# Kernel optimization log

Measured on AMD Instinct MI355X. Metric: run time of the kernel, lower is better.

Reference implementation:

```python
import jax, jax.numpy as jnp
import numpy as np

B, S, H, F, E, TOPK = 2, 1024, 1024, 2816, 8, 2

def setup_inputs() -> dict:
    key = jax.random.key(0)
    k1, k2, k3, k4 = jax.random.split(key, 4)
    return {
        "hidden_states": jax.random.normal(k1, (B, S, H), dtype=jnp.float32),
        "gate_w": jax.random.normal(k2, (E, H), dtype=jnp.float32) * 0.02,  # gate 1x1 conv == [E,H] matrix
        "w1": jax.random.normal(k3, (E, F, H), dtype=jnp.float32) * 0.02,   # per-expert up-proj
        "w2": jax.random.normal(k4, (E, H, F), dtype=jnp.float32) * 0.02,   # per-expert down-proj
        "top_k": TOPK,
    }

def reference(hidden_states, gate_w, w1, w2, top_k):
    b, s, h = hidden_states.shape
    e = gate_w.shape[0]
    x = hidden_states.reshape(-1, h)                       # [N, H]
    n = x.shape[0]
    # Router: 1x1 conv gate == linear, softmax, top-k, renormalize
    logits = x @ gate_w.T                                  # [N, E]
    probs = jax.nn.softmax(logits, axis=-1)
    topw, topi = jax.lax.top_k(probs, top_k)               # [N, k]
    topw = topw / jnp.sum(topw, axis=-1, keepdims=True)
    # Per-(token, expert) combine weight; zero for non-selected experts.
    # Equivalent to torch.where(topk_indices == e, topk_weights, 0).sum(-1).
    comb = jnp.zeros((n, e), dtype=x.dtype).at[jnp.arange(n)[:, None], topi].add(topw)  # [N, E]
    # Expert MLPs (1x1 convs == GEMMs): up -> SiLU -> down, weighted combine.
    up = jnp.einsum('nh,efh->nef', x, w1)                  # [N, E, F]
    act = jax.nn.silu(up)
    out = jnp.einsum('nef,ehf->neh', act, w2)              # [N, E, H]
    y = jnp.einsum('ne,neh->nh', comb, out)                # weighted combine
    return y.reshape(b, s, h)
```

## Files before the change

kernel.cpp:

```cpp
#include <hip/hip_runtime.h>
#include <hip/hip_bf16.h>
#include <stdint.h>

#define N_TOK 2048
#define H_DIM 1024
#define F_DIM 2816
#define N_EXP 8
#define NSLOT (N_TOK * 2)

#define BK 64
#define LDA 72
#define KSPLIT 2
#define KHALF (F_DIM / KSPLIT)

typedef __attribute__((ext_vector_type(8))) short bf16x8;
typedef __attribute__((ext_vector_type(4))) float f32x4;

static __device__ __forceinline__ unsigned short f2bf(float f) {
    union { float f; unsigned u; } v; v.f = f;
    unsigned r = v.u + 0x7fffu + ((v.u >> 16) & 1u);
    return (unsigned short)(r >> 16);
}

__global__ __launch_bounds__(256) void router_kernel(
    const float* __restrict__ x, const float* __restrict__ gate_w,
    int* __restrict__ counts, int* __restrict__ row_token, float* __restrict__ row_weight,
    int* __restrict__ slot_e, int* __restrict__ slot_pos)
{
    __shared__ float gsm[N_EXP * H_DIM];
    for (int i = threadIdx.x; i < N_EXP * H_DIM; i += 256) gsm[i] = gate_w[i];
    __syncthreads();

    const int wave = threadIdx.x >> 6;
    const int lane = threadIdx.x & 63;
    const int n = blockIdx.x * 4 + wave;
    if (n >= N_TOK) return;

    float xv[16];
#pragma unroll
    for (int i = 0; i < 16; i++) xv[i] = x[(size_t)n * H_DIM + lane + 64 * i];

    float logit[N_EXP];
#pragma unroll
    for (int e = 0; e < N_EXP; e++) {
        float p = 0.f;
#pragma unroll
        for (int i = 0; i < 16; i++) p += xv[i] * gsm[e * H_DIM + lane + 64 * i];
#pragma unroll
        for (int s = 32; s > 0; s >>= 1) p += __shfl_xor(p, s, 64);
        logit[e] = p;
    }

    if (lane == 0) {
        int e0 = 0; float l0 = logit[0];
#pragma unroll
        for (int e = 1; e < N_EXP; e++) if (logit[e] > l0) { l0 = logit[e]; e0 = e; }
        int e1 = -1; float l1 = -3.4e38f;
#pragma unroll
        for (int e = 0; e < N_EXP; e++) if (e != e0 && logit[e] > l1) { l1 = logit[e]; e1 = e; }
        float w0 = 1.f / (1.f + __expf(l1 - l0));
        float w1 = 1.f - w0;
        int p0 = atomicAdd(&counts[e0], 1);
        int p1 = atomicAdd(&counts[e1], 1);
        row_token[e0 * N_TOK + p0] = n;  row_weight[e0 * N_TOK + p0] = w0;
        row_token[e1 * N_TOK + p1] = n;  row_weight[e1 * N_TOK + p1] = w1;
        slot_e[n * 2 + 0] = e0;  slot_pos[n * 2 + 0] = p0;
        slot_e[n * 2 + 1] = e1;  slot_pos[n * 2 + 1] = p1;
    }
}

__global__ void scan_kernel(const int* __restrict__ counts, int* __restrict__ offsets)
{
    if (threadIdx.x == 0 && blockIdx.x == 0) {
        int acc = 0;
        for (int e = 0; e < N_EXP; e++) { offsets[e] = acc; acc += counts[e]; }
    }
}

__global__ __launch_bounds__(256, 2) void up_gemm_kernel(
    const float* __restrict__ x, const float* __restrict__ w1,
    const int* __restrict__ counts, const int* __restrict__ offsets,
    const int* __restrict__ row_token,
    unsigned short* __restrict__ act)
{
    const int e = blockIdx.z;
    const int cnt = counts[e];
    const int mTile = blockIdx.y;
    if (mTile * 128 >= cnt) return;
    const int fTile = blockIdx.x;
    const int off = offsets[e];

    __shared__ __align__(16) unsigned short As[2][128 * LDA];
    __shared__ __align__(16) unsigned short Bs[2][128 * LDA];

    const int tid = threadIdx.x;
    const int lane = tid & 63;
    const int wave = tid >> 6;
    const int wm = (wave >> 1) * 64, wn = (wave & 1) * 64;

    int tokens[8];
#pragma unroll
    for (int j = 0; j < 8; j++) {
        int i = tid + 256 * j;
        int row = i >> 4;
        int pos = mTile * 128 + row;
        tokens[j] = row_token[e * N_TOK + min(pos, cnt - 1)];
    }

    f32x4 acc[4][4];
#pragma unroll
    for (int i = 0; i < 4; i++)
#pragma unroll
        for (int j = 0; j < 4; j++) acc[i][j] = (f32x4)(0.f);

    const float* wbase = w1 + (size_t)e * F_DIM * H_DIM + (size_t)(fTile * 128) * H_DIM;

    float4 areg[8], breg[8];
#pragma unroll
    for (int j = 0; j < 8; j++) {
        int i = tid + 256 * j;
        int row = i >> 4, c = i & 15;
        areg[j] = *(const float4*)(x + (size_t)tokens[j] * H_DIM + c * 4);
        breg[j] = *(const float4*)(wbase + (size_t)row * H_DIM + c * 4);
    }

    const int NKT = H_DIM / BK;
    for (int kt = 0; kt < NKT; kt++) {
        const int cur = kt & 1;
#pragma unroll
        for (int j = 0; j < 8; j++) {
            int i = tid + 256 * j;
            int row = i >> 4, c = i & 15;
            float4 va = areg[j];
            ushort4 a4; a4.x = f2bf(va.x); a4.y = f2bf(va.y); a4.z = f2bf(va.z); a4.w = f2bf(va.w);
            *(ushort4*)(As[cur] + row * LDA + c * 4) = a4;
            float4 vb = breg[j];
            ushort4 b4; b4.x = f2bf(vb.x); b4.y = f2bf(vb.y); b4.z = f2bf(vb.z); b4.w = f2bf(vb.w);
            *(ushort4*)(Bs[cur] + row * LDA + c * 4) = b4;
        }
        __syncthreads();
        if (kt + 1 < NKT) {
            const int k0 = (kt + 1) * BK;
#pragma unroll
            for (int j = 0; j < 8; j++) {
                int i = tid + 256 * j;
                int row = i >> 4, c = i & 15;
                areg[j] = *(const float4*)(x + (size_t)tokens[j] * H_DIM + k0 + c * 4);
                breg[j] = *(const float4*)(wbase + (size_t)row * H_DIM + k0 + c * 4);
            }
        }
#pragma unroll
        for (int kk = 0; kk < BK / 32; kk++) {
            const int kloc = kk * 32 + (lane >> 4) * 8;
            bf16x8 af[4], bfr[4];
#pragma unroll
            for (int i = 0; i < 4; i++)
                af[i] = *(const bf16x8*)(As[cur] + (wm + i * 16 + (lane & 15)) * LDA + kloc);
#pragma unroll
            for (int i = 0; i < 4; i++)
                bfr[i] = *(const bf16x8*)(Bs[cur] + (wn + i * 16 + (lane & 15)) * LDA + kloc);
#pragma unroll
            for (int i = 0; i < 4; i++)
#pragma unroll
                for (int j = 0; j < 4; j++)
                    acc[i][j] = __builtin_amdgcn_mfma_f32_16x16x32_bf16(af[i], bfr[j], acc[i][j], 0, 0, 0);
        }
    }

#pragma unroll
    for (int i = 0; i < 4; i++) {
        const int mrow = wm + i * 16 + ((lane >> 4) << 2);
#pragma unroll
        for (int r = 0; r < 4; r++) {
            const int m = mTile * 128 + mrow + r;
            if (m < cnt) {
#pragma unroll
                for (int j = 0; j < 4; j++) {
                    float v = acc[i][j][r];
                    float s = v / (1.f + __expf(-v));
                    int col = fTile * 128 + wn + j * 16 + (lane & 15);
                    act[(size_t)(off + m) * F_DIM + col] = f2bf(s);
                }
            }
        }
    }
}

__global__ __launch_bounds__(256, 2) void down_gemm_kernel(
    const unsigned short* __restrict__ act, const float* __restrict__ w2,
    const int* __restrict__ counts, const int* __restrict__ offsets,
    const float* __restrict__ row_weight,
    float* __restrict__ out_partial)
{
    const int e  = blockIdx.z & (N_EXP - 1);
    const int ks = blockIdx.z >> 3;
    const int cnt = counts[e];
    const int mTile = blockIdx.y;
    if (mTile * 128 >= cnt) return;
    const int hTile = blockIdx.x;
    const int off = offsets[e];

    __shared__ __align__(16) unsigned short As[2][128 * LDA];
    __shared__ __align__(16) unsigned short Bs[2][128 * LDA];

    const int tid = threadIdx.x;
    const int lane = tid & 63;
    const int wave = tid >> 6;
    const int wm = (wave >> 1) * 64, wn = (wave & 1) * 64;

    int rowsg[4];
#pragma unroll
    for (int j = 0; j < 4; j++) {
        int i = tid + 256 * j;
        int row = i >> 3;
        rowsg[j] = off + min(mTile * 128 + row, cnt - 1);
    }

    f32x4 acc[4][4];
#pragma unroll
    for (int i = 0; i < 4; i++)
#pragma unroll
        for (int j = 0; j < 4; j++) acc[i][j] = (f32x4)(0.f);

    const float* wbase = w2 + (size_t)e * H_DIM * F_DIM + (size_t)(hTile * 128) * F_DIM;
    const int kbase = ks * KHALF;
    const int NKT = KHALF / BK;

    uint4 areg[4]; float4 breg[8];
#pragma unroll
    for (int j = 0; j < 4; j++) {
        int i = tid + 256 * j;
        int c = i & 7;
        areg[j] = *(const uint4*)(act + (size_t)rowsg[j] * F_DIM + kbase + c * 8);
    }
#pragma unroll
    for (int j = 0; j < 8; j++) {
        int i = tid + 256 * j;
        int row = i >> 4, c = i & 15;
        breg[j] = *(const float4*)(wbase + (size_t)row * F_DIM + kbase + c * 4);
    }

    for (int kt = 0; kt < NKT; kt++) {
        const int cur = kt & 1;
#pragma unroll
        for (int j = 0; j < 4; j++) {
            int i = tid + 256 * j;
            int row = i >> 3, c = i & 7;
            *(uint4*)(As[cur] + row * LDA + c * 8) = areg[j];
        }
#pragma unroll
        for (int j = 0; j < 8; j++) {
            int i = tid + 256 * j;
            int row = i >> 4, c = i & 15;
            float4 v = breg[j];
            ushort4 b4; b4.x = f2bf(v.x); b4.y = f2bf(v.y); b4.z = f2bf(v.z); b4.w = f2bf(v.w);
            *(ushort4*)(Bs[cur] + row * LDA + c * 4) = b4;
        }
        __syncthreads();
        if (kt + 1 < NKT) {
            const int k0 = kbase + (kt + 1) * BK;
#pragma unroll
            for (int j = 0; j < 4; j++) {
                int i = tid + 256 * j;
                int c = i & 7;
                areg[j] = *(const uint4*)(act + (size_t)rowsg[j] * F_DIM + k0 + c * 8);
            }
#pragma unroll
            for (int j = 0; j < 8; j++) {
                int i = tid + 256 * j;
                int row = i >> 4, c = i & 15;
                breg[j] = *(const float4*)(wbase + (size_t)row * F_DIM + k0 + c * 4);
            }
        }
#pragma unroll
        for (int kk = 0; kk < BK / 32; kk++) {
            const int kloc = kk * 32 + (lane >> 4) * 8;
            bf16x8 af[4], bfr[4];
#pragma unroll
            for (int i = 0; i < 4; i++)
                af[i] = *(const bf16x8*)(As[cur] + (wm + i * 16 + (lane & 15)) * LDA + kloc);
#pragma unroll
            for (int i = 0; i < 4; i++)
                bfr[i] = *(const bf16x8*)(Bs[cur] + (wn + i * 16 + (lane & 15)) * LDA + kloc);
#pragma unroll
            for (int i = 0; i < 4; i++)
#pragma unroll
                for (int j = 0; j < 4; j++)
                    acc[i][j] = __builtin_amdgcn_mfma_f32_16x16x32_bf16(af[i], bfr[j], acc[i][j], 0, 0, 0);
        }
    }

    float* obase = out_partial + (size_t)ks * NSLOT * H_DIM;
#pragma unroll
    for (int i = 0; i < 4; i++) {
        const int mrow = wm + i * 16 + ((lane >> 4) << 2);
#pragma unroll
        for (int r = 0; r < 4; r++) {
            const int m = mTile * 128 + mrow + r;
            if (m < cnt) {
                const float w = row_weight[e * N_TOK + m];
#pragma unroll
                for (int j = 0; j < 4; j++) {
                    int col = hTile * 128 + wn + j * 16 + (lane & 15);
                    obase[(size_t)(off + m) * H_DIM + col] = w * acc[i][j][r];
                }
            }
        }
    }
}

__global__ __launch_bounds__(256) void combine_kernel(
    const float* __restrict__ out_partial, const int* __restrict__ offsets,
    const int* __restrict__ slot_e, const int* __restrict__ slot_pos,
    float* __restrict__ out)
{
    const int n = blockIdx.x;
    const int r0 = offsets[slot_e[n * 2 + 0]] + slot_pos[n * 2 + 0];
    const int r1 = offsets[slot_e[n * 2 + 1]] + slot_pos[n * 2 + 1];
    const int t = threadIdx.x;
    const float* p0 = out_partial;
    const float* p1 = out_partial + (size_t)NSLOT * H_DIM;
    const float4 a = *(const float4*)(p0 + (size_t)r0 * H_DIM + t * 4);
    const float4 b = *(const float4*)(p1 + (size_t)r0 * H_DIM + t * 4);
    const float4 c = *(const float4*)(p0 + (size_t)r1 * H_DIM + t * 4);
    const float4 d = *(const float4*)(p1 + (size_t)r1 * H_DIM + t * 4);
    float4 s;
    s.x = (a.x + b.x) + (c.x + d.x);
    s.y = (a.y + b.y) + (c.y + d.y);
    s.z = (a.z + b.z) + (c.z + d.z);
    s.w = (a.w + b.w) + (c.w + d.w);
    *(float4*)(out + (size_t)n * H_DIM + t * 4) = s;
}

extern "C" void kernel_launch(void* const* d_in, const int* in_sizes, int n_in,
                              void* d_out, int out_size, void* d_ws, size_t ws_size,
                              hipStream_t stream) {
    const float* x      = (const float*)d_in[0];
    const float* gate_w = (const float*)d_in[1];
    const float* w1     = (const float*)d_in[2];
    const float* w2     = (const float*)d_in[3];
    float* out = (float*)d_out;

    char* ws = (char*)d_ws;
    size_t o = 0;
    auto alloc = [&](size_t bytes) -> void* {
        void* p = ws + o;
        o = (o + bytes + 255) & ~(size_t)255;
        return p;
    };
    int*   counts     = (int*)  alloc(N_EXP * sizeof(int));
    int*   offsets    = (int*)  alloc(N_EXP * sizeof(int));
    int*   row_token  = (int*)  alloc((size_t)N_EXP * N_TOK * sizeof(int));
    float* row_weight = (float*)alloc((size_t)N_EXP * N_TOK * sizeof(float));
    int*   slot_e     = (int*)  alloc((size_t)N_TOK * 2 * sizeof(int));
    int*   slot_pos   = (int*)  alloc((size_t)N_TOK * 2 * sizeof(int));
    unsigned short* act = (unsigned short*)alloc((size_t)NSLOT * F_DIM * sizeof(unsigned short));
    float* out_partial = (float*)alloc((size_t)KSPLIT * NSLOT * H_DIM * sizeof(float));

    hipMemsetAsync(counts, 0, N_EXP * sizeof(int), stream);

    router_kernel<<<N_TOK / 4, 256, 0, stream>>>(x, gate_w, counts, row_token, row_weight, slot_e, slot_pos);
    scan_kernel<<<1, 64, 0, stream>>>(counts, offsets);
    up_gemm_kernel<<<dim3(F_DIM / 128, N_TOK / 128, N_EXP), 256, 0, stream>>>(
        x, w1, counts, offsets, row_token, act);
    down_gemm_kernel<<<dim3(H_DIM / 128, N_TOK / 128, N_EXP * KSPLIT), 256, 0, stream>>>(
        act, w2, counts, offsets, row_weight, out_partial);
    combine_kernel<<<N_TOK, 256, 0, stream>>>(out_partial, offsets, slot_e, slot_pos, out);
}
```

Baseline: 447.3 us.

## Pre-convert inputs to bf16 and stage GEMM tiles via global_load_lds

Adds a conversion kernel that casts x, w1 and w2 to bf16 once per call into workspace buffers. The up and down GEMMs then copy bf16 tiles straight from global memory into LDS with the direct global-to-LDS load builtin, replacing register staging, in-loop conversion and double buffering. This removes per-tile conversion ALU work and halves weight bytes read inside the GEMMs. In exchange it adds a full pass over all weights every call, drops LDS padding (possible bank conflicts), and serialises loads and compute with two barriers per k-step.

```diff
diff --git a/kernel.cpp b/kernel.cpp
--- a/kernel.cpp
+++ b/kernel.cpp
@@ -1,5 +1,4 @@
 #include <hip/hip_runtime.h>
-#include <hip/hip_bf16.h>
 #include <stdint.h>
 
 #define N_TOK 2048
@@ -9,17 +8,52 @@
 #define NSLOT (N_TOK * 2)
 
 #define BK 64
-#define LDA 72
 #define KSPLIT 2
 #define KHALF (F_DIM / KSPLIT)
 
+#define N8_X (N_TOK * H_DIM / 8)
+#define N8_W (N_EXP * F_DIM * H_DIM / 8)
+
 typedef __attribute__((ext_vector_type(8))) short bf16x8;
 typedef __attribute__((ext_vector_type(4))) float f32x4;
+
+typedef __attribute__((address_space(1))) unsigned int gu32;
+typedef __attribute__((address_space(3))) unsigned int lu32;
 
 static __device__ __forceinline__ unsigned short f2bf(float f) {
     union { float f; unsigned u; } v; v.f = f;
     unsigned r = v.u + 0x7fffu + ((v.u >> 16) & 1u);
     return (unsigned short)(r >> 16);
+}
+
+static __device__ __forceinline__ void gload16(const unsigned short* g, unsigned short* l) {
+    __builtin_amdgcn_global_load_lds((const gu32*)g, (lu32*)l, 16, 0, 0);
+}
+
+__global__ __launch_bounds__(256) void convert_all_kernel(
+    const float* __restrict__ x, const float* __restrict__ w1, const float* __restrict__ w2,
+    unsigned short* __restrict__ x_bf, unsigned short* __restrict__ w1_bf, unsigned short* __restrict__ w2_bf)
+{
+    const int total = N8_X + 2 * N8_W;
+    int i = blockIdx.x * 256 + threadIdx.x;
+    const int stride = gridDim.x * 256;
+    for (; i < total; i += stride) {
+        const float* src; unsigned short* dst; size_t k;
+        if (i < N8_X)            { src = x;  dst = x_bf;  k = i; }
+        else if (i < N8_X + N8_W){ src = w1; dst = w1_bf; k = i - N8_X; }
+        else                     { src = w2; dst = w2_bf; k = i - N8_X - N8_W; }
+        const float4 a = *(const float4*)(src + k * 8);
+        const float4 b = *(const float4*)(src + k * 8 + 4);
+        ushort4 lo, hi;
+        lo.x = f2bf(a.x); lo.y = f2bf(a.y); lo.z = f2bf(a.z); lo.w = f2bf(a.w);
+        hi.x = f2bf(b.x); hi.y = f2bf(b.y); hi.z = f2bf(b.z); hi.w = f2bf(b.w);
+        uint4 out;
+        out.x = (unsigned)lo.x | ((unsigned)lo.y << 16);
+        out.y = (unsigned)lo.z | ((unsigned)lo.w << 16);
+        out.z = (unsigned)hi.x | ((unsigned)hi.y << 16);
+        out.w = (unsigned)hi.z | ((unsigned)hi.w << 16);
+        *(uint4*)(dst + k * 8) = out;
+    }
 }
 
 __global__ __launch_bounds__(256) void router_kernel(
@@ -77,8 +111,8 @@
     }
 }
 
-__global__ __launch_bounds__(256, 2) void up_gemm_kernel(
-    const float* __restrict__ x, const float* __restrict__ w1,
+__global__ __launch_bounds__(256) void up_gemm_kernel(
+    const unsigned short* __restrict__ x_bf, const unsigned short* __restrict__ w1_bf,
     const int* __restrict__ counts, const int* __restrict__ offsets,
     const int* __restrict__ row_token,
     unsigned short* __restrict__ act)
@@ -90,21 +124,23 @@
     const int fTile = blockIdx.x;
     const int off = offsets[e];
 
-    __shared__ __align__(16) unsigned short As[2][128 * LDA];
-    __shared__ __align__(16) unsigned short Bs[2][128 * LDA];
+    __shared__ __align__(16) unsigned short As[128 * 64];
+    __shared__ __align__(16) unsigned short Bs[128 * 64];
 
     const int tid = threadIdx.x;
     const int lane = tid & 63;
     const int wave = tid >> 6;
     const int wm = (wave >> 1) * 64, wn = (wave & 1) * 64;
 
-    int tokens[8];
-#pragma unroll
-    for (int j = 0; j < 8; j++) {
-        int i = tid + 256 * j;
-        int row = i >> 4;
-        int pos = mTile * 128 + row;
-        tokens[j] = row_token[e * N_TOK + min(pos, cnt - 1)];
+    const unsigned short* aSrc[4];
+    const unsigned short* bSrc[4];
+#pragma unroll
+    for (int j = 0; j < 4; j++) {
+        const int row_local = wave * 32 + j * 8 + (lane >> 3);
+        const int pos = mTile * 128 + row_local;
+        const int tok = row_token[e * N_TOK + min(pos, cnt - 1)];
+        aSrc[j] = x_bf + (size_t)tok * H_DIM + (lane & 7) * 8;
+        bSrc[j] = w1_bf + ((size_t)e * F_DIM + fTile * 128 + row_local) * H_DIM + (lane & 7) * 8;
     }
 
     f32x4 acc[4][4];
@@ -112,59 +148,33 @@
     for (int i = 0; i < 4; i++)
 #pragma unroll
         for (int j = 0; j < 4; j++) acc[i][j] = (f32x4)(0.f);
-
-    const float* wbase = w1 + (size_t)e * F_DIM * H_DIM + (size_t)(fTile * 128) * H_DIM;
-
-    float4 areg[8], breg[8];
-#pragma unroll
-    for (int j = 0; j < 8; j++) {
-        int i = tid + 256 * j;
-        int row = i >> 4, c = i & 15;
-        areg[j] = *(const float4*)(x + (size_t)tokens[j] * H_DIM + c * 4);
-        breg[j] = *(const float4*)(wbase + (size_t)row * H_DIM + c * 4);
-    }
 
     const int NKT = H_DIM / BK;
     for (int kt = 0; kt < NKT; kt++) {
-        const int cur = kt & 1;
-#pragma unroll
-        for (int j = 0; j < 8; j++) {
-            int i = tid + 256 * j;
-            int row = i >> 4, c = i & 15;
-            float4 va = areg[j];
-            ushort4 a4; a4.x = f2bf(va.x); a4.y = f2bf(va.y); a4.z = f2bf(va.z); a4.w = f2bf(va.w);
-            *(ushort4*)(As[cur] + row * LDA + c * 4) = a4;
-            float4 vb = breg[j];
-            ushort4 b4; b4.x = f2bf(vb.x); b4.y = f2bf(vb.y); b4.z = f2bf(vb.z); b4.w = f2bf(vb.w);
-            *(ushort4*)(Bs[cur] + row * LDA + c * 4) = b4;
+        const int koff = kt * BK;
+#pragma unroll
+        for (int j = 0; j < 4; j++) {
+            gload16(aSrc[j] + koff, As + (wave * 4 + j) * 512);
+            gload16(bSrc[j] + koff, Bs + (wave * 4 + j) * 512);
         }
         __syncthreads();
-        if (kt + 1 < NKT) {
-            const int k0 = (kt + 1) * BK;
-#pragma unroll
-            for (int j = 0; j < 8; j++) {
-                int i = tid + 256 * j;
-                int row = i >> 4, c = i & 15;
-                areg[j] = *(const float4*)(x + (size_t)tokens[j] * H_DIM + k0 + c * 4);
-                breg[j] = *(const float4*)(wbase + (size_t)row * H_DIM + k0 + c * 4);
-            }
-        }
 #pragma unroll
         for (int kk = 0; kk < BK / 32; kk++) {
             const int kloc = kk * 32 + (lane >> 4) * 8;
             bf16x8 af[4], bfr[4];
 #pragma unroll
             for (int i = 0; i < 4; i++)
-                af[i] = *(const bf16x8*)(As[cur] + (wm + i * 16 + (lane & 15)) * LDA + kloc);
-#pragma unroll
-            for (int i = 0; i < 4; i++)
-                bfr[i] = *(const bf16x8*)(Bs[cur] + (wn + i * 16 + (lane & 15)) * LDA + kloc);
+                af[i] = *(const bf16x8*)(As + (wm + i * 16 + (lane & 15)) * 64 + kloc);
+#pragma unroll
+            for (int i = 0; i < 4; i++)
+                bfr[i] = *(const bf16x8*)(Bs + (wn + i * 16 + (lane & 15)) * 64 + kloc);
 #pragma unroll
             for (int i = 0; i < 4; i++)
 #pragma unroll
                 for (int j = 0; j < 4; j++)
                     acc[i][j] = __builtin_amdgcn_mfma_f32_16x16x32_bf16(af[i], bfr[j], acc[i][j], 0, 0, 0);
         }
+        __syncthreads();
     }
 
 #pragma unroll
@@ -186,8 +196,8 @@
     }
 }
 
-__global__ __launch_bounds__(256, 2) void down_gemm_kernel(
-    const unsigned short* __restrict__ act, const float* __restrict__ w2,
+__global__ __launch_bounds__(256) void down_gemm_kernel(
+    const unsigned short* __restrict__ act, const unsigned short* __restrict__ w2_bf,
     const int* __restrict__ counts, const int* __restrict__ offsets,
     const float* __restrict__ row_weight,
     float* __restrict__ out_partial)
@@ -199,21 +209,24 @@
     if (mTile * 128 >= cnt) return;
     const int hTile = blockIdx.x;
     const int off = offsets[e];
-
-    __shared__ __align__(16) unsigned short As[2][128 * LDA];
-    __shared__ __align__(16) unsigned short Bs[2][128 * LDA];
+    const int kbase = ks * KHALF;
+
+    __shared__ __align__(16) unsigned short As[128 * 64];
+    __shared__ __align__(16) unsigned short Bs[128 * 64];
 
     const int tid = threadIdx.x;
     const int lane = tid & 63;
     const int wave = tid >> 6;
     const int wm = (wave >> 1) * 64, wn = (wave & 1) * 64;
 
-    int rowsg[4];
+    const unsigned short* aSrc[4];
+    const unsigned short* bSrc[4];
 #pragma unroll
     for (int j = 0; j < 4; j++) {
-        int i = tid + 256 * j;
-        int row = i >> 3;
-        rowsg[j] = off + min(mTile * 128 + row, cnt - 1);
+        const int row_local = wave * 32 + j * 8 + (lane >> 3);
+        const int slot = off + min(mTile * 128 + row_local, cnt - 1);
+        aSrc[j] = act + (size_t)slot * F_DIM + kbase + (lane & 7) * 8;
+        bSrc[j] = w2_bf + ((size_t)e * H_DIM + hTile * 128 + row_local) * F_DIM + kbase + (lane & 7) * 8;
     }
 
     f32x4 acc[4][4];
@@ -222,72 +235,32 @@
 #pragma unroll
         for (int j = 0; j < 4; j++) acc[i][j] = (f32x4)(0.f);
 
-    const float* wbase = w2 + (size_t)e * H_DIM * F_DIM + (size_t)(hTile * 128) * F_DIM;
-    const int kbase = ks * KHALF;
     const int NKT = KHALF / BK;
-
-    uint4 areg[4]; float4 breg[8];
-#pragma unroll
-    for (int j = 0; j < 4; j++) {
-        int i = tid + 256 * j;
-        int c = i & 7;
-        areg[j] = *(const uint4*)(act + (size_t)rowsg[j] * F_DIM + kbase + c * 8);
-    }
-#pragma unroll
-    for (int j = 0; j < 8; j++) {
-        int i = tid + 256 * j;
-        int row = i >> 4, c = i & 15;
-        breg[j] = *(const float4*)(wbase + (size_t)row * F_DIM + kbase + c * 4);
-    }
-
     for (int kt = 0; kt < NKT; kt++) {
-        const int cur = kt & 1;
+        const int koff = kt * BK;
 #pragma unroll
         for (int j = 0; j < 4; j++) {
-            int i = tid + 256 * j;
-            int row = i >> 3, c = i & 7;
-            *(uint4*)(As[cur] + row * LDA + c * 8) = areg[j];
-        }
-#pragma unroll
-        for (int j = 0; j < 8; j++) {
-            int i = tid + 256 * j;
-            int row = i >> 4, c = i & 15;
-            float4 v = breg[j];
-            ushort4 b4; b4.x = f2bf(v.x); b4.y = f2bf(v.y); b4.z = f2bf(v.z); b4.w = f2bf(v.w);
-            *(ushort4*)(Bs[cur] + row * LDA + c * 4) = b4;
+            gload16(aSrc[j] + koff, As + (wave * 4 + j) * 512);
+            gload16(bSrc[j] + koff, Bs + (wave * 4 + j) * 512);
         }
         __syncthreads();
-        if (kt + 1 < NKT) {
-            const int k0 = kbase + (kt + 1) * BK;
-#pragma unroll
-            for (int j = 0; j < 4; j++) {
-                int i = tid + 256 * j;
-                int c = i & 7;
-                areg[j] = *(const uint4*)(act + (size_t)rowsg[j] * F_DIM + k0 + c * 8);
-            }
-#pragma unroll
-            for (int j = 0; j < 8; j++) {
-                int i = tid + 256 * j;
-                int row = i >> 4, c = i & 15;
-                breg[j] = *(const float4*)(wbase + (size_t)row * F_DIM + k0 + c * 4);
-            }
-        }
 #pragma unroll
         for (int kk = 0; kk < BK / 32; kk++) {
             const int kloc = kk * 32 + (lane >> 4) * 8;
             bf16x8 af[4], bfr[4];
 #pragma unroll
             for (int i = 0; i < 4; i++)
-                af[i] = *(const bf16x8*)(As[cur] + (wm + i * 16 + (lane & 15)) * LDA + kloc);
-#pragma unroll
-            for (int i = 0; i < 4; i++)
-                bfr[i] = *(const bf16x8*)(Bs[cur] + (wn + i * 16 + (lane & 15)) * LDA + kloc);
+                af[i] = *(const bf16x8*)(As + (wm + i * 16 + (lane & 15)) * 64 + kloc);
+#pragma unroll
+            for (int i = 0; i < 4; i++)
+                bfr[i] = *(const bf16x8*)(Bs + (wn + i * 16 + (lane & 15)) * 64 + kloc);
 #pragma unroll
             for (int i = 0; i < 4; i++)
 #pragma unroll
                 for (int j = 0; j < 4; j++)
                     acc[i][j] = __builtin_amdgcn_mfma_f32_16x16x32_bf16(af[i], bfr[j], acc[i][j], 0, 0, 0);
         }
+        __syncthreads();
     }
 
     float* obase = out_partial + (size_t)ks * NSLOT * H_DIM;
@@ -356,14 +329,18 @@
     int*   slot_pos   = (int*)  alloc((size_t)N_TOK * 2 * sizeof(int));
     unsigned short* act = (unsigned short*)alloc((size_t)NSLOT * F_DIM * sizeof(unsigned short));
     float* out_partial = (float*)alloc((size_t)KSPLIT * NSLOT * H_DIM * sizeof(float));
+    unsigned short* x_bf  = (unsigned short*)alloc((size_t)N_TOK * H_DIM * sizeof(unsigned short));
+    unsigned short* w1_bf = (unsigned short*)alloc((size_t)N_EXP * F_DIM * H_DIM * sizeof(unsigned short));
+    unsigned short* w2_bf = (unsigned short*)alloc((size_t)N_EXP * H_DIM * F_DIM * sizeof(unsigned short));
 
     hipMemsetAsync(counts, 0, N_EXP * sizeof(int), stream);
 
     router_kernel<<<N_TOK / 4, 256, 0, stream>>>(x, gate_w, counts, row_token, row_weight, slot_e, slot_pos);
     scan_kernel<<<1, 64, 0, stream>>>(counts, offsets);
+    convert_all_kernel<<<2048, 256, 0, stream>>>(x, w1, w2, x_bf, w1_bf, w2_bf);
     up_gemm_kernel<<<dim3(F_DIM / 128, N_TOK / 128, N_EXP), 256, 0, stream>>>(
-        x, w1, counts, offsets, row_token, act);
+        x_bf, w1_bf, counts, offsets, row_token, act);
     down_gemm_kernel<<<dim3(H_DIM / 128, N_TOK / 128, N_EXP * KSPLIT), 256, 0, stream>>>(
-        act, w2, counts, offsets, row_weight, out_partial);
+        act, w2_bf, counts, offsets, row_weight, out_partial);
     combine_kernel<<<N_TOK, 256, 0, stream>>>(out_partial, offsets, slot_e, slot_pos, out);
 }
```

Result: faster. 391.7 us (-12.4%).
